# Performance work log

Hardware: AMD Instinct MI355X
Metric: run time of the kernel (lower is better)

The kernel has to match this reference:

```python
import jax, jax.numpy as jnp
import numpy as np

B = 262144      # batch
N = 64          # input_size (PCS size)
P = 8           # output_size // input_size = number of PCS submodules


def setup_inputs() -> dict:
    key = jax.random.key(0)
    k1, k2 = jax.random.split(key)
    x = jax.random.normal(k1, (B, N), dtype=jnp.float32)
    # Each PCS has its own 2-element weightParameter -> stacked [P, 2]
    w = jax.random.normal(k2, (P, 2), dtype=jnp.float32)
    # distinct_permutations of [0,1,1,...,1]: row i has 0 at position i, 1 elsewhere
    indices = (1 - jnp.eye(N, dtype=jnp.int32))
    return {"x": x, "w": w, "indices": indices}


def reference(x, w, indices):
    # Gather the shared weights into full [P, N, N] permutation-symmetric matrices
    W = w[:, indices]                       # [P, N, N]
    # Each PCS: x @ W_p.T ; hstack over PCS -> [B, P*N]
    out = jnp.einsum('bn,pmn->bpm', x, W)   # [B, P, N]
    return out.reshape(x.shape[0], -1)      # [B, P*N]
```

## Files before the change

kernel.cpp:

```cpp
#include <hip/hip_runtime.h>


constexpr int BROWS   = 262144;
constexpr int N       = 64;
constexpr int P       = 8;
constexpr int ROWS    = 16;
constexpr int THREADS = 256;

__global__ __launch_bounds__(THREADS)
void pcl_kernel(const float* __restrict__ x,
                const float* __restrict__ w,
                float* __restrict__ out)
{
    __shared__ float4 sx[ROWS][N / 4];
    __shared__ float  ssum[ROWS];
    __shared__ float  sd[P];
    __shared__ float  sw1[P];

    const int t = threadIdx.x;
    const long long rowBase = (long long)blockIdx.x * ROWS;

    if (t < P) {
        float w0 = w[2 * t];
        float w1 = w[2 * t + 1];
        sd[t]  = w0 - w1;
        sw1[t] = w1;
    }

    const float4* x4 = (const float4*)(x + rowBase * N);
    float4 v = x4[t];
    const int r = t >> 4;
    sx[r][t & 15] = v;

    float partial = v.x + v.y + v.z + v.w;
    #pragma unroll
    for (int m = 8; m >= 1; m >>= 1)
        partial += __shfl_xor(partial, m, 16);
    if ((t & 15) == 0) ssum[r] = partial;

    __syncthreads();

    float4* out4 = (float4*)(out + rowBase * (long long)(P * N));
    #pragma unroll
    for (int j = 0; j < 8; ++j) {
        const int idx4 = j * THREADS + t;
        const int rr = idx4 >> 7;
        const int o  = idx4 & 127;
        const int p  = o >> 4;
        const int ms = o & 15;
        const float4 xv = sx[rr][ms];
        const float  S  = ssum[rr];
        const float  d  = sd[p];
        const float  w1 = sw1[p];
        float4 ov;
        ov.x = xv.x * d + w1 * S;
        ov.y = xv.y * d + w1 * S;
        ov.z = xv.z * d + w1 * S;
        ov.w = xv.w * d + w1 * S;
        out4[idx4] = ov;
    }
}

extern "C" void kernel_launch(void* const* d_in, const int* in_sizes, int n_in,
                              void* d_out, int out_size, void* d_ws, size_t ws_size,
                              hipStream_t stream)
{
    const float* x = (const float*)d_in[0];
    const float* w = (const float*)d_in[1];
    float* out = (float*)d_out;

    pcl_kernel<<<BROWS / ROWS, THREADS, 0, stream>>>(x, w, out);
}
```

Measured before the change: 573.7 us.

## Use persistent grid-stride register kernel with nontemporal loads and stores

Replaces the shared-memory staged kernel with a fixed grid of 2048 blocks. Each thread loads 8 strided float4 chunks of x up front using nontemporal loads, reduces row sums via 16-lane shuffles, and writes the 8 output projections directly with nontemporal stores. This removes the LDS staging and __syncthreads, and gives each thread more memory-level parallelism. The trade-offs are that each thread's stores are spread across 8 p-slices (16 float4 apart per lane group), and that every thread redundantly loads the weights.

After: 572.9 us. About the same (-0.1%).

```diff
diff --git a/kernel.cpp b/kernel.cpp
--- a/kernel.cpp
+++ b/kernel.cpp
@@ -1,63 +1,62 @@
 #include <hip/hip_runtime.h>
 
+
+typedef float f4 __attribute__((ext_vector_type(4)));
 
 constexpr int BROWS   = 262144;
 constexpr int N       = 64;
 constexpr int P       = 8;
-constexpr int ROWS    = 16;
 constexpr int THREADS = 256;
+constexpr int BLOCKS  = 2048;
+constexpr int UNROLL  = 8;
+static_assert((long long)BLOCKS * THREADS * UNROLL ==
+              (long long)BROWS * N / 4, "grid must tile x exactly");
 
 __global__ __launch_bounds__(THREADS)
-void pcl_kernel(const float* __restrict__ x,
+void pcl_kernel(const f4* __restrict__ x4,
                 const float* __restrict__ w,
-                float* __restrict__ out)
+                f4* __restrict__ out4)
 {
-    __shared__ float4 sx[ROWS][N / 4];
-    __shared__ float  ssum[ROWS];
-    __shared__ float  sd[P];
-    __shared__ float  sw1[P];
+    float d[P], w1[P];
+    #pragma unroll
+    for (int p = 0; p < P; ++p) {
+        const float a = w[2 * p];
+        const float b = w[2 * p + 1];
+        d[p]  = a - b;
+        w1[p] = b;
+    }
 
     const int t = threadIdx.x;
-    const long long rowBase = (long long)blockIdx.x * ROWS;
+    const long long base   = (long long)blockIdx.x * THREADS + t;
+    constexpr long long STRIDE = (long long)BLOCKS * THREADS;
 
-    if (t < P) {
-        float w0 = w[2 * t];
-        float w1 = w[2 * t + 1];
-        sd[t]  = w0 - w1;
-        sw1[t] = w1;
-    }
+    f4 v[UNROLL];
+    #pragma unroll
+    for (int k = 0; k < UNROLL; ++k)
+        v[k] = __builtin_nontemporal_load(&x4[base + (long long)k * STRIDE]);
 
-    const float4* x4 = (const float4*)(x + rowBase * N);
-    float4 v = x4[t];
-    const int r = t >> 4;
-    sx[r][t & 15] = v;
+    #pragma unroll
+    for (int k = 0; k < UNROLL; ++k) {
+        const long long i = base + (long long)k * STRIDE;
+        float s = v[k].x + v[k].y + v[k].z + v[k].w;
+        s += __shfl_xor(s, 1, 16);
+        s += __shfl_xor(s, 2, 16);
+        s += __shfl_xor(s, 4, 16);
+        s += __shfl_xor(s, 8, 16);
 
-    float partial = v.x + v.y + v.z + v.w;
-    #pragma unroll
-    for (int m = 8; m >= 1; m >>= 1)
-        partial += __shfl_xor(partial, m, 16);
-    if ((t & 15) == 0) ssum[r] = partial;
-
-    __syncthreads();
-
-    float4* out4 = (float4*)(out + rowBase * (long long)(P * N));
-    #pragma unroll
-    for (int j = 0; j < 8; ++j) {
-        const int idx4 = j * THREADS + t;
-        const int rr = idx4 >> 7;
-        const int o  = idx4 & 127;
-        const int p  = o >> 4;
-        const int ms = o & 15;
-        const float4 xv = sx[rr][ms];
-        const float  S  = ssum[rr];
-        const float  d  = sd[p];
-        const float  w1 = sw1[p];
-        float4 ov;
-        ov.x = xv.x * d + w1 * S;
-        ov.y = xv.y * d + w1 * S;
-        ov.z = xv.z * d + w1 * S;
-        ov.w = xv.w * d + w1 * S;
-        out4[idx4] = ov;
+        const long long r  = i >> 4;
+        const int       ms = (int)(i & 15);
+        f4* op = out4 + r * 128 + ms;
+        #pragma unroll
+        for (int p = 0; p < P; ++p) {
+            const float bb = w1[p] * s;
+            f4 o;
+            o.x = v[k].x * d[p] + bb;
+            o.y = v[k].y * d[p] + bb;
+            o.z = v[k].z * d[p] + bb;
+            o.w = v[k].w * d[p] + bb;
+            __builtin_nontemporal_store(o, op + p * 16);
+        }
     }
 }
 
@@ -65,9 +64,9 @@
                               void* d_out, int out_size, void* d_ws, size_t ws_size,
                               hipStream_t stream)
 {
-    const float* x = (const float*)d_in[0];
+    const f4* x = (const f4*)d_in[0];
     const float* w = (const float*)d_in[1];
-    float* out = (float*)d_out;
+    f4* out = (f4*)d_out;
 
-    pcl_kernel<<<BROWS / ROWS, THREADS, 0, stream>>>(x, w, out);
+    pcl_kernel<<<BLOCKS, THREADS, 0, stream>>>(x, w, out);
 }
```
